# Kernel optimization log

Measured on AMD Instinct MI355X. Metric: run time of the kernel, lower is better.

Reference implementation:

```python
import jax, jax.numpy as jnp
import numpy as np

N_GENE, N_TRAIN, N_EDGES = 20000, 4096, 131072
SRC, DST, H, OUT, NC = 2500, 2675, 2500, 2500, 16
EPS = 1e-5
SLOPE = 0.01  # torch default leaky_relu negative slope


def _leaky(x):
    return jnp.where(x >= 0, x, SLOPE * x)


def _bn(x, g, b):
    # BatchNorm1d, training-mode batch statistics over the node (batch) dim
    m = x.mean(axis=0)
    v = x.var(axis=0)
    return (x - m) * jax.lax.rsqrt(v + EPS) * g + b


def _ln(x, g, b):
    m = x.mean(axis=-1, keepdims=True)
    v = x.var(axis=-1, keepdims=True)
    return (x - m) * jax.lax.rsqrt(v + EPS) * g + b


def _sage(src_f, dst_f, si, di, W_self, W_neigh, b, n_dst):
    # DGL SAGEConv 'mean': fc_self(h_dst) + fc_neigh(mean over in-neighbors)
    msg = src_f[si]                                            # [E, d_src] gather
    agg = jax.ops.segment_sum(msg, di, num_segments=n_dst)     # [n_dst, d_src]
    deg = jax.ops.segment_sum(jnp.ones((si.shape[0],), src_f.dtype), di, num_segments=n_dst)
    mean = agg / jnp.maximum(deg, 1.0)[:, None]
    return dst_f @ W_self + mean @ W_neigh + b


def setup_inputs() -> dict:
    key = jax.random.key(0)
    ks = jax.random.split(key, 20)
    s = 0.02  # weight scale to keep deep 2500-dim chain numerically tame
    n = lambda k, shp: jax.random.normal(k, shp, dtype=jnp.float32)
    return {
        'gene_feats': n(ks[0], (N_GENE, SRC)),
        'train_feats': n(ks[1], (N_TRAIN, DST - NC)),
        'y_hat': n(ks[2], (N_TRAIN, NC)),
        'edge_src': jax.random.randint(ks[3], (N_EDGES,), 0, N_GENE, dtype=jnp.int32),
        'edge_dst': jax.random.randint(ks[4], (N_EDGES,), 0, N_TRAIN, dtype=jnp.int32),
        'W_self3': n(ks[5], (DST, H)) * s, 'W_neigh3': n(ks[6], (SRC, H)) * s, 'b3': jnp.zeros((H,), jnp.float32),
        'bn3_g': jnp.ones((H,), jnp.float32), 'bn3_b': jnp.zeros((H,), jnp.float32),
        'Wq': n(ks[7], (H, H)) * s, 'Wk': n(ks[8], (H, H)) * s, 'Wv': n(ks[9], (H, H)) * s,
        'bq': jnp.zeros((H,), jnp.float32), 'bk': jnp.zeros((H,), jnp.float32), 'bv': jnp.zeros((H,), jnp.float32),
        'Wo': n(ks[10], (H, H)) * s, 'bo': jnp.zeros((H,), jnp.float32),
        'ln2_g': jnp.ones((H,), jnp.float32), 'ln2_b': jnp.zeros((H,), jnp.float32),
        'W_self4': n(ks[11], (H, OUT)) * s, 'W_neigh4': n(ks[12], (SRC, OUT)) * s, 'b4': jnp.zeros((OUT,), jnp.float32),
        'bn4_g': jnp.ones((OUT,), jnp.float32), 'bn4_b': jnp.zeros((OUT,), jnp.float32),
        'W_lin2': n(ks[13], (OUT, OUT)) * s, 'b_lin2': jnp.zeros((OUT,), jnp.float32),
        'W_ce': n(ks[14], (OUT, NC)) * s, 'b_ce': jnp.zeros((NC,), jnp.float32),
    }


def reference(gene_feats, train_feats, y_hat, edge_src, edge_dst,
              W_self3, W_neigh3, b3, bn3_g, bn3_b,
              Wq, Wk, Wv, bq, bk, bv, Wo, bo, ln2_g, ln2_b,
              W_self4, W_neigh4, b4, bn4_g, bn4_b,
              W_lin2, b_lin2, W_ce, b_ce):
    # concat label logits onto train-node features (dst dim -> 2675)
    dst = jnp.concatenate([train_feats, y_hat], axis=1)
    # conv3: bipartite SAGE gene_node -> train_node
    h = _sage(gene_feats, dst, edge_src, edge_dst, W_self3, W_neigh3, b3, N_TRAIN)
    h = _leaky(_bn(h, bn3_g, bn3_b))
    # single-head self-attention over ALL train nodes as one sequence [L=N_TRAIN, E=H]
    q = h @ Wq + bq
    k = h @ Wk + bk
    v = h @ Wv + bv
    attn = jax.nn.softmax(q @ k.T * (1.0 / jnp.sqrt(jnp.asarray(H, h.dtype))), axis=-1)
    h = (attn @ v) @ Wo + bo
    h = _leaky(_ln(h, ln2_g, ln2_b))
    # (dropout omitted: eval-mode identity)
    # conv4: same graph, src = raw gene feats, dst = attention output
    h = _sage(gene_feats, h, edge_src, edge_dst, W_self4, W_neigh4, b4, N_TRAIN)
    x_hat = _leaky(_bn(h, bn4_g, bn4_b))
    y = jax.nn.relu(x_hat @ W_lin2 + b_lin2) @ W_ce + b_ce
    return (x_hat, y)
```

## Files before the change

### kernel.cpp

```cpp
#include <hip/hip_runtime.h>
#include <hip/hip_bf16.h>
#include <cstdint>
#include <cstddef>

constexpr int NTRAIN = 4096;
constexpr int NEDGES = 131072;
constexpr int DSRC = 2500, DH = 2500, DNC = 16;
constexpr int KD1 = 2659;
constexpr int KC3 = 5175;
constexpr int KP3 = 5184;
constexpr int KC4 = 5000;
constexpr int KP4 = 5056;
constexpr int KPH = 2560;
constexpr int NPW = 2560;
constexpr int NQKV = 7680;
constexpr int GSTR = 2504;
constexpr float EPSV = 1e-5f;
constexpr float SLOPEV = 0.01f;

typedef __attribute__((ext_vector_type(8))) short bf16x8;
typedef __attribute__((ext_vector_type(4))) float f32x4;

static __device__ __forceinline__ unsigned short bfbits(float f) {
    __hip_bfloat16 h = __float2bfloat16(f);
    return *reinterpret_cast<unsigned short*>(&h);
}
static __device__ __forceinline__ float b2f(short s) {
    return __uint_as_float(((unsigned)(unsigned short)s) << 16);
}

__global__ void count_deg_k(const int* __restrict__ edst, int* __restrict__ deg) {
    int e = blockIdx.x * 256 + threadIdx.x;
    if (e < NEDGES) atomicAdd(&deg[edst[e]], 1);
}

__global__ __launch_bounds__(1024) void scan_deg_k(const int* __restrict__ deg,
                                                   int* __restrict__ indptr,
                                                   int* __restrict__ cursor) {
    __shared__ int sums[1024];
    int t = threadIdx.x;
    int base = t * 4;
    int d0 = deg[base + 0], d1 = deg[base + 1], d2 = deg[base + 2], d3 = deg[base + 3];
    sums[t] = d0 + d1 + d2 + d3;
    __syncthreads();
    for (int o = 1; o < 1024; o <<= 1) {
        int v = (t >= o) ? sums[t - o] : 0;
        __syncthreads();
        sums[t] += v;
        __syncthreads();
    }
    int excl = (t == 0) ? 0 : sums[t - 1];
    int p0 = excl, p1 = p0 + d0, p2 = p1 + d1, p3 = p2 + d2;
    indptr[base + 0] = p0; indptr[base + 1] = p1; indptr[base + 2] = p2; indptr[base + 3] = p3;
    cursor[base + 0] = p0; cursor[base + 1] = p1; cursor[base + 2] = p2; cursor[base + 3] = p3;
    if (t == 1023) indptr[4096] = p3 + d3;
}

__global__ void scatter_edges_k(const int* __restrict__ esrc, const int* __restrict__ edst,
                                int* __restrict__ cursor, int* __restrict__ csr_src) {
    int e = blockIdx.x * 256 + threadIdx.x;
    if (e < NEDGES) {
        int d = edst[e];
        int p = atomicAdd(&cursor[d], 1);
        csr_src[p] = esrc[e];
    }
}

__global__ __launch_bounds__(256) void gene2bf_k(const float* __restrict__ gene,
                                                 short* __restrict__ gbf) {
    int v = blockIdx.x * 256 + threadIdx.x;
    if (v >= 313) return;
    int row = blockIdx.y;
    const float* src = gene + (size_t)row * DSRC + v * 8;
    f32x4 a = *(const f32x4*)(src);
    f32x4 b = {0.f, 0.f, 0.f, 0.f};
    if (v < 312) b = *(const f32x4*)(src + 4);
    bf16x8 o;
#pragma unroll
    for (int c = 0; c < 4; c++) o[c] = (short)bfbits(a[c]);
#pragma unroll
    for (int c = 0; c < 4; c++) o[4 + c] = (short)bfbits(b[c]);
    *(bf16x8*)(gbf + (size_t)row * GSTR + v * 8) = o;
}

__global__ __launch_bounds__(256) void sage_mean_k(const short* __restrict__ gbf,
                                                   const int* __restrict__ indptr,
                                                   const int* __restrict__ csr_src,
                                                   __hip_bfloat16* __restrict__ A3,
                                                   __hip_bfloat16* __restrict__ A4) {
    int row = blockIdx.x;
    int s = indptr[row], e = indptr[row + 1];
    int t = threadIdx.x;
    float a0[8], a1[8];
#pragma unroll
    for (int c = 0; c < 8; c++) { a0[c] = 0.f; a1[c] = 0.f; }
    bool has1 = (t < 57);
    int j = s;
    for (; j + 2 <= e; j += 2) {
        const bf16x8* g0 = (const bf16x8*)(gbf + (size_t)csr_src[j] * GSTR);
        const bf16x8* g1 = (const bf16x8*)(gbf + (size_t)csr_src[j + 1] * GSTR);
        bf16x8 u0 = g0[t], w0 = g1[t];
        bf16x8 u1, w1;
        if (has1) { u1 = g0[t + 256]; w1 = g1[t + 256]; }
#pragma unroll
        for (int c = 0; c < 8; c++) a0[c] += b2f(u0[c]) + b2f(w0[c]);
        if (has1) {
#pragma unroll
            for (int c = 0; c < 8; c++) a1[c] += b2f(u1[c]) + b2f(w1[c]);
        }
    }
    if (j < e) {
        const bf16x8* g0 = (const bf16x8*)(gbf + (size_t)csr_src[j] * GSTR);
        bf16x8 u0 = g0[t];
#pragma unroll
        for (int c = 0; c < 8; c++) a0[c] += b2f(u0[c]);
        if (has1) {
            bf16x8 u1 = g0[t + 256];
#pragma unroll
            for (int c = 0; c < 8; c++) a1[c] += b2f(u1[c]);
        }
    }
    float inv = 1.f / fmaxf((float)(e - s), 1.f);
#pragma unroll
    for (int c = 0; c < 8; c++) {
        int f = t * 8 + c;
        __hip_bfloat16 h = __float2bfloat16(a0[c] * inv);
        A3[(size_t)row * KP3 + 2675 + f] = h;
        A4[(size_t)row * KP4 + 2500 + f] = h;
    }
    if (has1) {
#pragma unroll
        for (int c = 0; c < 8; c++) {
            int f = (t + 256) * 8 + c;
            if (f < 2500) {
                __hip_bfloat16 h = __float2bfloat16(a1[c] * inv);
                A3[(size_t)row * KP3 + 2675 + f] = h;
                A4[(size_t)row * KP4 + 2500 + f] = h;
            }
        }
    }
}

__global__ void dst_build_k(const float* __restrict__ trainf, const float* __restrict__ yhat,
                            __hip_bfloat16* __restrict__ A3) {
    int c = blockIdx.x * 256 + threadIdx.x;
    int r = blockIdx.y;
    if (c >= KP3) return;
    if (c >= 2675 && c < KC3) return;
    float v = 0.f;
    if (c < KD1) v = trainf[(size_t)r * KD1 + c];
    else if (c < 2675) v = yhat[r * DNC + (c - KD1)];
    A3[(size_t)r * KP3 + c] = __float2bfloat16(v);
}

__global__ __launch_bounds__(256) void wtrans_k(const float* __restrict__ W1,
                                                const float* __restrict__ W2, int ldw,
                                                __hip_bfloat16* __restrict__ Wt,
                                                int Nreal, int K1, int K12, int Kpad, int Npad) {
    __shared__ float tile[32][33];
    int k0 = blockIdx.x * 32, n0 = blockIdx.y * 32;
    int x = threadIdx.x & 31, y = threadIdx.x >> 5;
#pragma unroll
    for (int i = 0; i < 32; i += 8) {
        int k = k0 + y + i, n = n0 + x;
        float v = 0.f;
        if (n < Nreal) {
            if (k < K1) v = W1[(size_t)k * ldw + n];
            else if (k < K12) v = W2[(size_t)(k - K1) * ldw + n];
        }
        tile[y + i][x] = v;
    }
    __syncthreads();
#pragma unroll
    for (int i = 0; i < 32; i += 8) {
        int n = n0 + y + i, k = k0 + x;
        if (n < Npad && k < Kpad) Wt[(size_t)n * Kpad + k] = __float2bfloat16(tile[x][y + i]);
    }
}

__global__ __launch_bounds__(256) void btrans_k(const __hip_bfloat16* __restrict__ V, int ldv,
                                                __hip_bfloat16* __restrict__ VT) {
    __shared__ __hip_bfloat16 tile[32][33];
    int r0 = blockIdx.x * 32, c0 = blockIdx.y * 32;
    int x = threadIdx.x & 31, y = threadIdx.x >> 5;
#pragma unroll
    for (int i = 0; i < 32; i += 8)
        tile[y + i][x] = V[(size_t)(r0 + y + i) * ldv + c0 + x];
    __syncthreads();
#pragma unroll
    for (int i = 0; i < 32; i += 8)
        VT[(size_t)(c0 + y + i) * NTRAIN + r0 + x] = tile[x][y + i];
}

__global__ void qkv_bias_k(const float* __restrict__ bq, const float* __restrict__ bk,
                           const float* __restrict__ bv, float* __restrict__ bqkv) {
    int i = blockIdx.x * 256 + threadIdx.x;
    if (i >= NQKV) return;
    int j = i / KPH, c = i % KPH;
    const float* src = (j == 0) ? bq : (j == 1) ? bk : bv;
    bqkv[i] = (c < DH) ? src[c] : 0.f;
}

__device__ __forceinline__ void async_cp16(const void* g, void* l) {
    __builtin_amdgcn_global_load_lds((const __attribute__((address_space(1))) void*)g,
                                     (__attribute__((address_space(3))) void*)l, 16, 0, 0);
}
#define WAITVM(N) asm volatile("s_waitcnt vmcnt(" #N ")" ::: "memory")
#define LGKM0 asm volatile("s_waitcnt lgkmcnt(0)" ::: "memory")
#define SB __builtin_amdgcn_sched_barrier(0)
static __device__ __forceinline__ void bar_raw() {
    asm volatile("" ::: "memory");
    __builtin_amdgcn_s_barrier();
    asm volatile("" ::: "memory");
}

__global__ __launch_bounds__(512, 2) void gemm256_k(const short* __restrict__ A,
                                                    const short* __restrict__ Bt,
                                                    const float* __restrict__ bias,
                                                    float* __restrict__ Cf,
                                                    __hip_bfloat16* __restrict__ Cb,
                                                    float* __restrict__ psOut,
                                                    float* __restrict__ ps2Out,
                                                    int N, int K, int sA, int sB, int ldc,
                                                    int nmod, float alpha, int act) {
    __shared__ short smem[65536];
    int nwg = gridDim.x * gridDim.y;
    int orig = blockIdx.y * gridDim.x + blockIdx.x;
    int qd = nwg >> 3, rr = nwg & 7;
    int xcd = orig & 7, oidx = orig >> 3;
    int nb = (xcd < rr ? xcd * (qd + 1) : rr * (qd + 1) + (xcd - rr) * qd) + oidx;
    int bx = nb % gridDim.x, by = nb / gridDim.x;
    int row0 = by * 256, col0 = bx * 256;

    int tid = threadIdx.x;
    int wave = tid >> 6, lane = tid & 63;
    int wm = wave >> 2, wn = wave & 3;

    int rsub = lane >> 2;
    int cs = ((lane & 3) * 8) ^ ((lane >= 32) ? 16 : 0);
    const short* gA0 = A + (size_t)(row0 + wave * 16 + rsub) * sA + cs;
    const short* gA1 = A + (size_t)(row0 + wave * 16 + 128 + rsub) * sA + cs;
    const short* gB0 = Bt + (size_t)(col0 + wave * 16 + rsub) * sB + cs;
    const short* gB1 = Bt + (size_t)(col0 + wave * 16 + 128 + rsub) * sB + cs;
    int sa0 = wave * 1024;
    int sa1 = (wave + 8) * 1024;

    int fr = lane & 15, kq = lane >> 4;
    int roff = fr * 32 + ((kq * 8) ^ ((fr & 8) ? 16 : 0));

    f32x4 acc[8][4];
#pragma unroll
    for (int i = 0; i < 8; i++)
#pragma unroll
        for (int j = 0; j < 4; j++)
#pragma unroll
            for (int r = 0; r < 4; r++) acc[i][j][r] = 0.f;

#define STAGE_A(kb, b, k0s) { \
    short* l0 = smem + (b) * 32768 + sa0 + (kb) * 512; \
    short* l1 = smem + (b) * 32768 + sa1 + (kb) * 512; \
    async_cp16(gA0 + (k0s) + (kb) * 32, l0); \
    async_cp16(gA1 + (k0s) + (kb) * 32, l1); }
#define STAGE_B(kb, b, k0s) { \
    short* l0 = smem + (b) * 32768 + 16384 + sa0 + (kb) * 512; \
    short* l1 = smem + (b) * 32768 + 16384 + sa1 + (kb) * 512; \
    async_cp16(gB0 + (k0s) + (kb) * 32, l0); \
    async_cp16(gB1 + (k0s) + (kb) * 32, l1); }
#define DSRA(dst, mq, kk) \
    _Pragma("unroll") for (int i = 0; i < 4; i++) \
        dst[i] = *(const bf16x8*)(ab + (((wm * 8 + (mq) * 4 + i) * 2 + (kk)) << 9) + roff);
#define DSRB(dst, kk) \
    _Pragma("unroll") for (int j = 0; j < 4; j++) \
        dst[j] = *(const bf16x8*)(bb + (((wn * 4 + j) * 2 + (kk)) << 9) + roff);
#define MFMA16(av, bvv, mq) \
    __builtin_amdgcn_s_setprio(1); \
    _Pragma("unroll") for (int i = 0; i < 4; i++) \
        _Pragma("unroll") for (int j = 0; j < 4; j++) \
            acc[(mq) * 4 + i][j] = __builtin_amdgcn_mfma_f32_16x16x32_bf16(av[i], bvv[j], acc[(mq) * 4 + i][j], 0, 0, 0); \
    __builtin_amdgcn_s_setprio(0);

    int nt = K >> 6;
    STAGE_A(0, 0, 0); STAGE_B(0, 0, 0); STAGE_A(1, 0, 0); STAGE_B(1, 0, 0);
    WAITVM(4);
    bar_raw();
    int buf = 0;
    for (int t = 0; t < nt - 1; ++t) {
        const short* ab = smem + (buf << 15);
        const short* bb = ab + 16384;
        int k1 = (t + 1) << 6;
        bf16x8 a0[4], a1[4], b0[4], b1[4];
        DSRA(a0, 0, 0); DSRB(b0, 0);
        STAGE_A(0, buf ^ 1, k1);
        bar_raw(); LGKM0; SB;
        MFMA16(a0, b0, 0);
        SB; bar_raw();
        DSRA(a1, 1, 0);
        STAGE_B(0, buf ^ 1, k1);
        WAITVM(4);
        bar_raw(); LGKM0; SB;
        MFMA16(a1, b0, 1);
        SB; bar_raw();
        DSRA(a0, 0, 1); DSRB(b1, 1);
        STAGE_A(1, buf ^ 1, k1);
        bar_raw(); LGKM0; SB;
        MFMA16(a0, b1, 0);
        SB; bar_raw();
        DSRA(a1, 1, 1);
        STAGE_B(1, buf ^ 1, k1);
        WAITVM(4);
        bar_raw(); LGKM0; SB;
        MFMA16(a1, b1, 1);
        SB; bar_raw();
        buf ^= 1;
    }
    {
        const short* ab = smem + (buf << 15);
        const short* bb = ab + 16384;
        bf16x8 a0[4], a1[4], b0[4], b1[4];
        DSRA(a0, 0, 0); DSRB(b0, 0);
        bar_raw(); LGKM0; SB;
        MFMA16(a0, b0, 0);
        SB; bar_raw();
        DSRA(a1, 1, 0);
        WAITVM(0);
        bar_raw(); LGKM0; SB;
        MFMA16(a1, b0, 1);
        SB; bar_raw();
        DSRA(a0, 0, 1); DSRB(b1, 1);
        bar_raw(); LGKM0; SB;
        MFMA16(a0, b1, 0);
        SB; bar_raw();
        DSRA(a1, 1, 1);
        bar_raw(); LGKM0; SB;
        MFMA16(a1, b1, 1);
        SB;
    }
#undef STAGE_A
#undef STAGE_B
#undef DSRA
#undef DSRB
#undef MFMA16

    int cn = lane & 15, cm = kq * 4;
    int mbase = row0 + wm * 128, nbase = col0 + wn * 64;
    if (Cb) {
#pragma unroll
        for (int j = 0; j < 4; j++) {
            int n = nbase + j * 16 + cn;
            if (n >= ldc) continue;
            bool real = (n % nmod) < N;
            float bvv = (real && bias) ? bias[n] : 0.f;
#pragma unroll
            for (int i = 0; i < 8; i++) {
#pragma unroll
                for (int r = 0; r < 4; r++) {
                    int m = mbase + i * 16 + cm + r;
                    float c = real ? alpha * acc[i][j][r] + bvv : 0.f;
                    if (act) c = fmaxf(c, 0.f);
                    Cb[(size_t)m * ldc + n] = __float2bfloat16(c);
                }
            }
        }
    } else {
#pragma unroll
        for (int j = 0; j < 4; j++) {
            int n = nbase + j * 16 + cn;
            if (n >= N) continue;
            float bvv = bias ? bias[n] : 0.f;
#pragma unroll
            for (int i = 0; i < 8; i++) {
#pragma unroll
                for (int r = 0; r < 4; r++) {
                    int m = mbase + i * 16 + cm + r;
                    float c = alpha * acc[i][j][r] + bvv;
                    if (act) c = fmaxf(c, 0.f);
                    Cf[(size_t)m * ldc + n] = c;
                }
            }
        }
    }
    if (!Cb && psOut) {
        float cs[4], cs2[4];
#pragma unroll
        for (int j = 0; j < 4; j++) { cs[j] = 0.f; cs2[j] = 0.f; }
#pragma unroll
        for (int j = 0; j < 4; j++) {
            int n = nbase + j * 16 + cn;
            if (n >= N) continue;
            float bvv = bias ? bias[n] : 0.f;
#pragma unroll
            for (int i = 0; i < 8; i++) {
#pragma unroll
                for (int r = 0; r < 4; r++) {
                    float c = alpha * acc[i][j][r] + bvv;
                    if (act) c = fmaxf(c, 0.f);
                    cs[j] += c;
                    cs2[j] += c * c;
                }
            }
        }
        bar_raw();
        float* red = (float*)smem;
        int pid = wm * 4 + kq;
#pragma unroll
        for (int j = 0; j < 4; j++) {
            int slot = wn * 64 + j * 16 + cn;
            red[pid * 256 + slot] = cs[j];
            red[2048 + pid * 256 + slot] = cs2[j];
        }
        bar_raw();
        if (wm == 0 && kq == 0) {
#pragma unroll
            for (int j = 0; j < 4; j++) {
                int slot = wn * 64 + j * 16 + cn;
                float s = 0.f, s2 = 0.f;
#pragma unroll
                for (int p = 0; p < 8; p++) {
                    s += red[p * 256 + slot];
                    s2 += red[2048 + p * 256 + slot];
                }
                int n = col0 + slot;
                if (n < N) {
                    psOut[(size_t)by * N + n] = s;
                    ps2Out[(size_t)by * N + n] = s2;
                }
            }
        }
    }
}

__global__ void bn_finalize_k(const float* __restrict__ ps, const float* __restrict__ ps2,
                              const float* __restrict__ g, const float* __restrict__ b,
                              float* __restrict__ scale, float* __restrict__ shift,
                              int Ncol, int nParts, int M) {
    int c = blockIdx.x * 256 + threadIdx.x;
    if (c >= Ncol) return;
    double s = 0, s2 = 0;
    for (int p = 0; p < nParts; p++) {
        s += ps[(size_t)p * Ncol + c];
        s2 += ps2[(size_t)p * Ncol + c];
    }
    double m = s / M;
    double v = s2 / M - m * m;
    float sc = g[c] / sqrtf((float)v + EPSV);
    scale[c] = sc;
    shift[c] = b[c] - (float)m * sc;
}

__global__ void bn_apply_k(const float* __restrict__ X, const float* __restrict__ scale,
                           const float* __restrict__ shift, __hip_bfloat16* __restrict__ Yb,
                           float* __restrict__ Yf, int Nreal, int Cpad) {
    int c = blockIdx.x * 256 + threadIdx.x;
    int r = blockIdx.y;
    if (c >= Cpad) return;
    float v = 0.f;
    if (c < Nreal) {
        v = fmaf(X[(size_t)r * Nreal + c], scale[c], shift[c]);
        v = v >= 0.f ? v : SLOPEV * v;
        if (Yf) Yf[(size_t)r * Nreal + c] = v;
    }
    Yb[(size_t)r * Cpad + c] = __float2bfloat16(v);
}

__device__ __forceinline__ double wave_sum_d(double v) {
#pragma unroll
    for (int o = 32; o > 0; o >>= 1) v += __shfl_down(v, o, 64);
    return v;
}
__device__ __forceinline__ float wave_sum_f(float v) {
#pragma unroll
    for (int o = 32; o > 0; o >>= 1) v += __shfl_down(v, o, 64);
    return v;
}
__device__ __forceinline__ float wave_max_f(float v) {
#pragma unroll
    for (int o = 32; o > 0; o >>= 1) v = fmaxf(v, __shfl_down(v, o, 64));
    return v;
}

__global__ __launch_bounds__(256) void ln_leaky_k(const float* __restrict__ X,
                                                  const float* __restrict__ g,
                                                  const float* __restrict__ b,
                                                  __hip_bfloat16* __restrict__ A4) {
    int row = blockIdx.x;
    const float* xr = X + (size_t)row * DH;
    double s = 0, s2 = 0;
    for (int c = threadIdx.x; c < DH; c += 256) {
        float x = xr[c];
        s += x;
        s2 += (double)x * x;
    }
    __shared__ double sb[4], sb2[4];
    int lane = threadIdx.x & 63, w = threadIdx.x >> 6;
    s = wave_sum_d(s);
    s2 = wave_sum_d(s2);
    if (lane == 0) { sb[w] = s; sb2[w] = s2; }
    __syncthreads();
    double S = sb[0] + sb[1] + sb[2] + sb[3];
    double S2 = sb2[0] + sb2[1] + sb2[2] + sb2[3];
    double m = S / DH;
    double v = S2 / DH - m * m;
    float inv = 1.f / sqrtf((float)v + EPSV);
    float mf = (float)m;
    __hip_bfloat16* yr = A4 + (size_t)row * KP4;
    for (int c = threadIdx.x; c < DH; c += 256) {
        float x = (xr[c] - mf) * inv * g[c] + b[c];
        x = x >= 0.f ? x : SLOPEV * x;
        yr[c] = __float2bfloat16(x);
    }
    if (threadIdx.x < KP4 - KC4) yr[KC4 + threadIdx.x] = __float2bfloat16(0.f);
}

__global__ __launch_bounds__(256) void softmax1_k(const float* __restrict__ X,
                                                  __hip_bfloat16* __restrict__ Y) {
    int row = blockIdx.x, t = threadIdx.x;
    const f32x4* xr = reinterpret_cast<const f32x4*>(X + (size_t)row * NTRAIN);
    f32x4 v[4];
    float mx = -3.4e38f;
#pragma unroll
    for (int i = 0; i < 4; i++) {
        v[i] = xr[i * 256 + t];
#pragma unroll
        for (int c = 0; c < 4; c++) mx = fmaxf(mx, v[i][c]);
    }
    __shared__ float sb[4];
    int lane = t & 63, w = t >> 6;
    mx = wave_max_f(mx);
    if (lane == 0) sb[w] = mx;
    __syncthreads();
    mx = fmaxf(fmaxf(sb[0], sb[1]), fmaxf(sb[2], sb[3]));
    float s = 0.f;
#pragma unroll
    for (int i = 0; i < 4; i++)
#pragma unroll
        for (int c = 0; c < 4; c++) {
            float e = expf(v[i][c] - mx);
            v[i][c] = e;
            s += e;
        }
    s = wave_sum_f(s);
    __syncthreads();
    if (lane == 0) sb[w] = s;
    __syncthreads();
    float inv = 1.f / (sb[0] + sb[1] + sb[2] + sb[3]);
    ushort4* yr = reinterpret_cast<ushort4*>(Y + (size_t)row * NTRAIN);
#pragma unroll
    for (int i = 0; i < 4; i++) {
        ushort4 o;
        o.x = bfbits(v[i][0] * inv);
        o.y = bfbits(v[i][1] * inv);
        o.z = bfbits(v[i][2] * inv);
        o.w = bfbits(v[i][3] * inv);
        yr[i * 256 + t] = o;
    }
}

__global__ __launch_bounds__(256) void head_k(const float* __restrict__ X,
                                              const float* __restrict__ Wce,
                                              const float* __restrict__ bce,
                                              float* __restrict__ Y) {
    int row = blockIdx.x;
    int n = threadIdx.x & 15, part = threadIdx.x >> 4;
    const float* xr = X + (size_t)row * DH;
    float s = 0.f;
    for (int k = part; k < DH; k += 16) s += xr[k] * Wce[k * 16 + n];
    __shared__ float red[256];
    red[threadIdx.x] = s;
    __syncthreads();
    for (int off = 8; off >= 1; off >>= 1) {
        if (part < off) red[threadIdx.x] += red[threadIdx.x + off * 16];
        __syncthreads();
    }
    if (part == 0) Y[row * 16 + n] = red[n] + bce[n];
}

extern "C" void kernel_launch(void* const* d_in, const int* in_sizes, int n_in,
                              void* d_out, int out_size, void* d_ws, size_t ws_size,
                              hipStream_t stream) {
    const float* gene    = (const float*)d_in[0];
    const float* trainf  = (const float*)d_in[1];
    const float* yhat    = (const float*)d_in[2];
    const int*   esrc    = (const int*)d_in[3];
    const int*   edst    = (const int*)d_in[4];
    const float* W_self3 = (const float*)d_in[5];
    const float* W_neigh3= (const float*)d_in[6];
    const float* b3      = (const float*)d_in[7];
    const float* bn3_g   = (const float*)d_in[8];
    const float* bn3_b   = (const float*)d_in[9];
    const float* Wq      = (const float*)d_in[10];
    const float* Wk      = (const float*)d_in[11];
    const float* Wv      = (const float*)d_in[12];
    const float* bq      = (const float*)d_in[13];
    const float* bk      = (const float*)d_in[14];
    const float* bv      = (const float*)d_in[15];
    const float* Wo      = (const float*)d_in[16];
    const float* bo      = (const float*)d_in[17];
    const float* ln2_g   = (const float*)d_in[18];
    const float* ln2_b   = (const float*)d_in[19];
    const float* W_self4 = (const float*)d_in[20];
    const float* W_neigh4= (const float*)d_in[21];
    const float* b4      = (const float*)d_in[22];
    const float* bn4_g   = (const float*)d_in[23];
    const float* bn4_b   = (const float*)d_in[24];
    const float* W_lin2  = (const float*)d_in[25];
    const float* b_lin2  = (const float*)d_in[26];
    const float* W_ce    = (const float*)d_in[27];
    const float* b_ce    = (const float*)d_in[28];

    char* ws = (char*)d_ws;
    size_t off = 0;
    auto alloc = [&](size_t bytes) -> void* {
        void* p = ws + off;
        off = (off + bytes + 255) & ~(size_t)255;
        return p;
    };
    __hip_bfloat16* A3cat  = (__hip_bfloat16*)alloc((size_t)NTRAIN * KP3 * 2);
    __hip_bfloat16* A4cat  = (__hip_bfloat16*)alloc((size_t)NTRAIN * KP4 * 2);
    __hip_bfloat16* h_bf   = (__hip_bfloat16*)alloc((size_t)NTRAIN * KPH * 2);
    __hip_bfloat16* qkv_bf = (__hip_bfloat16*)alloc((size_t)NTRAIN * NQKV * 2);
    __hip_bfloat16* W3t    = (__hip_bfloat16*)alloc((size_t)NPW * KP3 * 2);
    __hip_bfloat16* Wqkvt  = (__hip_bfloat16*)alloc((size_t)3 * NPW * KPH * 2);
    float*  bigC   = (float*)alloc((size_t)NTRAIN * NTRAIN * 4);
    float*  ps     = (float*)alloc((size_t)16 * DH * 4);
    float*  ps2    = (float*)alloc((size_t)16 * DH * 4);
    float*  scale  = (float*)alloc(DH * 4);
    float*  shift  = (float*)alloc(DH * 4);
    float*  bqkv   = (float*)alloc(NQKV * 4);
    int*    deg    = (int*)alloc(NTRAIN * 4);
    int*    indptr = (int*)alloc((NTRAIN + 1) * 4);
    int*    cursor = (int*)alloc(NTRAIN * 4);
    int*    csr_src= (int*)alloc(NEDGES * 4);
    __hip_bfloat16* attn_bf = A3cat;
    __hip_bfloat16* W4t     = W3t;
    __hip_bfloat16* Wot     = Wqkvt;
    __hip_bfloat16* Wlin2t  = Wqkvt;
    __hip_bfloat16* xhat_bf = h_bf;
    __hip_bfloat16* ao_bf   = qkv_bf;
    __hip_bfloat16* vT_bf   = (__hip_bfloat16*)bigC;
    short* gene_bf = (short*)W3t;

    float* xhat = (float*)d_out;
    float* yout = (float*)d_out + (size_t)NTRAIN * DH;

    auto gemm = [&](const void* A, const void* Bt, const float* bias, float* Cf,
                    __hip_bfloat16* Cb, float* psO, float* ps2O, int NpadCols, int Nreal,
                    int K, int sA, int sB, int ldc, int nmod, float alpha, int act) {
        dim3 g(NpadCols / 256, NTRAIN / 256);
        gemm256_k<<<g, 512, 0, stream>>>((const short*)A, (const short*)Bt, bias, Cf, Cb,
                                         psO, ps2O, Nreal, K, sA, sB, ldc, nmod, alpha, act);
    };

    hipMemsetAsync(deg, 0, NTRAIN * 4, stream);
    count_deg_k<<<NEDGES / 256, 256, 0, stream>>>(edst, deg);
    scan_deg_k<<<1, 1024, 0, stream>>>(deg, indptr, cursor);
    scatter_edges_k<<<NEDGES / 256, 256, 0, stream>>>(esrc, edst, cursor, csr_src);
    gene2bf_k<<<dim3(2, 20000), 256, 0, stream>>>(gene, gene_bf);
    sage_mean_k<<<NTRAIN, 256, 0, stream>>>(gene_bf, indptr, csr_src, A3cat, A4cat);
    dst_build_k<<<dim3((KP3 + 255) / 256, NTRAIN), 256, 0, stream>>>(trainf, yhat, A3cat);
    wtrans_k<<<dim3(KP3 / 32, NPW / 32), 256, 0, stream>>>(W_self3, W_neigh3, DH, W3t, DH, 2675, KC3, KP3, NPW);

    gemm(A3cat, W3t, b3, bigC, nullptr, ps, ps2, NPW, DH, KP3, KP3, KP3, DH, DH, 1.f, 0);
    bn_finalize_k<<<(DH + 255) / 256, 256, 0, stream>>>(ps, ps2, bn3_g, bn3_b, scale, shift, DH, 16, NTRAIN);
    bn_apply_k<<<dim3((KPH + 255) / 256, NTRAIN), 256, 0, stream>>>(bigC, scale, shift, h_bf, nullptr, DH, KPH);

    wtrans_k<<<dim3(KPH / 32, NPW / 32), 256, 0, stream>>>(Wq, nullptr, DH, Wqkvt, DH, DH, DH, KPH, NPW);
    wtrans_k<<<dim3(KPH / 32, NPW / 32), 256, 0, stream>>>(Wk, nullptr, DH, Wqkvt + (size_t)NPW * KPH, DH, DH, DH, KPH, NPW);
    wtrans_k<<<dim3(KPH / 32, NPW / 32), 256, 0, stream>>>(Wv, nullptr, DH, Wqkvt + (size_t)2 * NPW * KPH, DH, DH, DH, KPH, NPW);
    qkv_bias_k<<<NQKV / 256, 256, 0, stream>>>(bq, bk, bv, bqkv);
    gemm(h_bf, Wqkvt, bqkv, nullptr, qkv_bf, nullptr, nullptr, NQKV, DH, KPH, KPH, KPH, NQKV, KPH, 1.f, 0);
    gemm(qkv_bf, qkv_bf + KPH, nullptr, bigC, nullptr, nullptr, nullptr, NTRAIN, NTRAIN, KPH, NQKV, NQKV, NTRAIN, NTRAIN, 0.02f, 0);
    softmax1_k<<<NTRAIN, 256, 0, stream>>>(bigC, attn_bf);
    btrans_k<<<dim3(NTRAIN / 32, KPH / 32), 256, 0, stream>>>(qkv_bf + 2 * KPH, NQKV, vT_bf);
    gemm(attn_bf, vT_bf, nullptr, nullptr, ao_bf, nullptr, nullptr, NPW, DH, NTRAIN, NTRAIN, NTRAIN, KPH, KPH, 1.f, 0);
    wtrans_k<<<dim3(KPH / 32, NPW / 32), 256, 0, stream>>>(Wo, nullptr, DH, Wot, DH, DH, DH, KPH, NPW);
    gemm(ao_bf, Wot, bo, bigC, nullptr, nullptr, nullptr, NPW, DH, KPH, KPH, KPH, DH, DH, 1.f, 0);
    ln_leaky_k<<<NTRAIN, 256, 0, stream>>>(bigC, ln2_g, ln2_b, A4cat);

    wtrans_k<<<dim3(KP4 / 32, NPW / 32), 256, 0, stream>>>(W_self4, W_neigh4, DH, W4t, DH, DH, KC4, KP4, NPW);
    gemm(A4cat, W4t, b4, bigC, nullptr, ps, ps2, NPW, DH, KP4, KP4, KP4, DH, DH, 1.f, 0);
    bn_finalize_k<<<(DH + 255) / 256, 256, 0, stream>>>(ps, ps2, bn4_g, bn4_b, scale, shift, DH, 16, NTRAIN);
    bn_apply_k<<<dim3((KPH + 255) / 256, NTRAIN), 256, 0, stream>>>(bigC, scale, shift, xhat_bf, xhat, DH, KPH);

    wtrans_k<<<dim3(KPH / 32, NPW / 32), 256, 0, stream>>>(W_lin2, nullptr, DH, Wlin2t, DH, DH, DH, KPH, NPW);
    gemm(xhat_bf, Wlin2t, b_lin2, bigC, nullptr, nullptr, nullptr, NPW, DH, KPH, KPH, KPH, DH, DH, 1.f, 1);
    head_k<<<NTRAIN, 256, 0, stream>>>(bigC, W_ce, b_ce, yout);
    (void)ws_size; (void)n_in; (void)in_sizes; (void)out_size;
}
```

Baseline: 1.674 ms.

## Fold weight transposes into preceding GEMM launches as extra workgroups

The separate weight-transpose/bf16-convert kernels (Wq/Wk/Wv, Wo, W4, W_lin2) are removed. Their work now runs as extra workgroups appended to an earlier, independent GEMM launch. Those blocks take a branch at kernel entry and do tiled transposes through LDS. This is meant to remove launch overhead and let the transposes fill the GEMM tail. The risks are more kernel arguments, possible register or occupancy effects, and the need for the aliased scratch buffers to be free when they are written.

```diff
diff --git a/kernel.cpp b/kernel.cpp
--- a/kernel.cpp
+++ b/kernel.cpp
@@ -222,10 +222,54 @@
                                                     float* __restrict__ psOut,
                                                     float* __restrict__ ps2Out,
                                                     int N, int K, int sA, int sB, int ldc,
-                                                    int nmod, float alpha, int act) {
+                                                    int nmod, float alpha, int act,
+                                                    int ngemm,
+                                                    const float* xs0, const float* xs1,
+                                                    const float* xs2, const float* xs3,
+                                                    const float* xs4, const float* xs5,
+                                                    short* xout, long xstride,
+                                                    int xldw, int xNreal, int xK1, int xK12,
+                                                    int xKpad, int xNpad, int nslab) {
     __shared__ short smem[65536];
-    int nwg = gridDim.x * gridDim.y;
+    int nwgt = gridDim.x * gridDim.y;
     int orig = blockIdx.y * gridDim.x + blockIdx.x;
+
+    if (orig >= ngemm) {
+        int wid = orig - ngemm, nw = nwgt - ngemm;
+        float* tile = (float*)smem;
+        int tid = threadIdx.x;
+        int x = tid & 31, y0 = tid >> 5;
+        int ntx = xKpad >> 5, nty = xNpad >> 5;
+        int per = ntx * nty, total = nslab * per;
+        for (int t = wid; t < total; t += nw) {
+            int sl = t / per, rem = t - sl * per;
+            int tx = rem % ntx, ty = rem / ntx;
+            const float* W1 = (sl == 0) ? xs0 : (sl == 1) ? xs2 : xs4;
+            const float* W2 = (sl == 0) ? xs1 : (sl == 1) ? xs3 : xs5;
+            short* out = xout + (size_t)sl * xstride;
+            int k0 = tx * 32, n0 = ty * 32;
+            __syncthreads();
+#pragma unroll
+            for (int i = 0; i < 32; i += 16) {
+                int k = k0 + y0 + i, n = n0 + x;
+                float v = 0.f;
+                if (n < xNreal) {
+                    if (k < xK1) v = W1[(size_t)k * xldw + n];
+                    else if (k < xK12) v = W2[(size_t)(k - xK1) * xldw + n];
+                }
+                tile[(y0 + i) * 33 + x] = v;
+            }
+            __syncthreads();
+#pragma unroll
+            for (int i = 0; i < 32; i += 16) {
+                int n = n0 + y0 + i, k = k0 + x;
+                out[(size_t)n * xKpad + k] = (short)bfbits(tile[x * 33 + y0 + i]);
+            }
+        }
+        return;
+    }
+
+    int nwg = ngemm;
     int qd = nwg >> 3, rr = nwg & 7;
     int xcd = orig & 7, oidx = orig >> 3;
     int nb = (xcd < rr ? xcd * (qd + 1) : rr * (qd + 1) + (xcd - rr) * qd) + oidx;
@@ -380,9 +424,9 @@
         }
     }
     if (!Cb && psOut) {
-        float cs[4], cs2[4];
-#pragma unroll
-        for (int j = 0; j < 4; j++) { cs[j] = 0.f; cs2[j] = 0.f; }
+        float cs2v[4], cs1v[4];
+#pragma unroll
+        for (int j = 0; j < 4; j++) { cs1v[j] = 0.f; cs2v[j] = 0.f; }
 #pragma unroll
         for (int j = 0; j < 4; j++) {
             int n = nbase + j * 16 + cn;
@@ -394,8 +438,8 @@
                 for (int r = 0; r < 4; r++) {
                     float c = alpha * acc[i][j][r] + bvv;
                     if (act) c = fmaxf(c, 0.f);
-                    cs[j] += c;
-                    cs2[j] += c * c;
+                    cs1v[j] += c;
+                    cs2v[j] += c * c;
                 }
             }
         }
@@ -405,8 +449,8 @@
 #pragma unroll
         for (int j = 0; j < 4; j++) {
             int slot = wn * 64 + j * 16 + cn;
-            red[pid * 256 + slot] = cs[j];
-            red[2048 + pid * 256 + slot] = cs2[j];
+            red[pid * 256 + slot] = cs1v[j];
+            red[2048 + pid * 256 + slot] = cs2v[j];
         }
         bar_raw();
         if (wm == 0 && kq == 0) {
@@ -644,11 +688,20 @@
 
     auto gemm = [&](const void* A, const void* Bt, const float* bias, float* Cf,
                     __hip_bfloat16* Cb, float* psO, float* ps2O, int NpadCols, int Nreal,
-                    int K, int sA, int sB, int ldc, int nmod, float alpha, int act) {
-        dim3 g(NpadCols / 256, NTRAIN / 256);
+                    int K, int sA, int sB, int ldc, int nmod, float alpha, int act,
+                    const float* x0, const float* x1, const float* x2, const float* x3,
+                    const float* x4, const float* x5, short* xout, long xstride,
+                    int xldw, int xNreal, int xK1, int xK12, int xKpad, int xNpad, int nslab) {
+        int gx = NpadCols / 256, gy = NTRAIN / 256;
+        int ngemm = gx * gy;
+        int extraY = (nslab > 0) ? 9 : 0;
+        dim3 g(gx, gy + extraY);
         gemm256_k<<<g, 512, 0, stream>>>((const short*)A, (const short*)Bt, bias, Cf, Cb,
-                                         psO, ps2O, Nreal, K, sA, sB, ldc, nmod, alpha, act);
+                                         psO, ps2O, Nreal, K, sA, sB, ldc, nmod, alpha, act,
+                                         ngemm, x0, x1, x2, x3, x4, x5, xout, xstride,
+                                         xldw, xNreal, xK1, xK12, xKpad, xNpad, nslab);
     };
+    const float* Z = nullptr;
 
     hipMemsetAsync(deg, 0, NTRAIN * 4, stream);
     count_deg_k<<<NEDGES / 256, 256, 0, stream>>>(edst, deg);
@@ -659,30 +712,31 @@
     dst_build_k<<<dim3((KP3 + 255) / 256, NTRAIN), 256, 0, stream>>>(trainf, yhat, A3cat);
     wtrans_k<<<dim3(KP3 / 32, NPW / 32), 256, 0, stream>>>(W_self3, W_neigh3, DH, W3t, DH, 2675, KC3, KP3, NPW);
 
-    gemm(A3cat, W3t, b3, bigC, nullptr, ps, ps2, NPW, DH, KP3, KP3, KP3, DH, DH, 1.f, 0);
+    gemm(A3cat, W3t, b3, bigC, nullptr, ps, ps2, NPW, DH, KP3, KP3, KP3, DH, DH, 1.f, 0,
+         Wq, Z, Wk, Z, Wv, Z, (short*)Wqkvt, (long)NPW * KPH, DH, DH, DH, DH, KPH, NPW, 3);
     bn_finalize_k<<<(DH + 255) / 256, 256, 0, stream>>>(ps, ps2, bn3_g, bn3_b, scale, shift, DH, 16, NTRAIN);
     bn_apply_k<<<dim3((KPH + 255) / 256, NTRAIN), 256, 0, stream>>>(bigC, scale, shift, h_bf, nullptr, DH, KPH);
 
-    wtrans_k<<<dim3(KPH / 32, NPW / 32), 256, 0, stream>>>(Wq, nullptr, DH, Wqkvt, DH, DH, DH, KPH, NPW);
-    wtrans_k<<<dim3(KPH / 32, NPW / 32), 256, 0, stream>>>(Wk, nullptr, DH, Wqkvt + (size_t)NPW * KPH, DH, DH, DH, KPH, NPW);
-    wtrans_k<<<dim3(KPH / 32, NPW / 32), 256, 0, stream>>>(Wv, nullptr, DH, Wqkvt + (size_t)2 * NPW * KPH, DH, DH, DH, KPH, NPW);
     qkv_bias_k<<<NQKV / 256, 256, 0, stream>>>(bq, bk, bv, bqkv);
-    gemm(h_bf, Wqkvt, bqkv, nullptr, qkv_bf, nullptr, nullptr, NQKV, DH, KPH, KPH, KPH, NQKV, KPH, 1.f, 0);
-    gemm(qkv_bf, qkv_bf + KPH, nullptr, bigC, nullptr, nullptr, nullptr, NTRAIN, NTRAIN, KPH, NQKV, NQKV, NTRAIN, NTRAIN, 0.02f, 0);
+    gemm(h_bf, Wqkvt, bqkv, nullptr, qkv_bf, nullptr, nullptr, NQKV, DH, KPH, KPH, KPH, NQKV, KPH, 1.f, 0,
+         Z, Z, Z, Z, Z, Z, nullptr, 0, 0, 0, 0, 0, 32, 32, 0);
+    gemm(qkv_bf, qkv_bf + KPH, nullptr, bigC, nullptr, nullptr, nullptr, NTRAIN, NTRAIN, KPH, NQKV, NQKV, NTRAIN, NTRAIN, 0.02f, 0,
+         Z, Z, Z, Z, Z, Z, nullptr, 0, 0, 0, 0, 0, 32, 32, 0);
     softmax1_k<<<NTRAIN, 256, 0, stream>>>(bigC, attn_bf);
     btrans_k<<<dim3(NTRAIN / 32, KPH / 32), 256, 0, stream>>>(qkv_bf + 2 * KPH, NQKV, vT_bf);
-    gemm(attn_bf, vT_bf, nullptr, nullptr, ao_bf, nullptr, nullptr, NPW, DH, NTRAIN, NTRAIN, NTRAIN, KPH, KPH, 1.f, 0);
-    wtrans_k<<<dim3(KPH / 32, NPW / 32), 256, 0, stream>>>(Wo, nullptr, DH, Wot, DH, DH, DH, KPH, NPW);
-    gemm(ao_bf, Wot, bo, bigC, nullptr, nullptr, nullptr, NPW, DH, KPH, KPH, KPH, DH, DH, 1.f, 0);
+    gemm(attn_bf, vT_bf, nullptr, nullptr, ao_bf, nullptr, nullptr, NPW, DH, NTRAIN, NTRAIN, NTRAIN, KPH, KPH, 1.f, 0,
+         Wo, Z, Z, Z, Z, Z, (short*)Wot, 0, DH, DH, DH, DH, KPH, NPW, 1);
+    gemm(ao_bf, Wot, bo, bigC, nullptr, nullptr, nullptr, NPW, DH, KPH, KPH, KPH, DH, DH, 1.f, 0,
+         W_self4, W_neigh4, Z, Z, Z, Z, (short*)W4t, 0, DH, DH, DH, KC4, KP4, NPW, 1);
     ln_leaky_k<<<NTRAIN, 256, 0, stream>>>(bigC, ln2_g, ln2_b, A4cat);
 
-    wtrans_k<<<dim3(KP4 / 32, NPW / 32), 256, 0, stream>>>(W_self4, W_neigh4, DH, W4t, DH, DH, KC4, KP4, NPW);
-    gemm(A4cat, W4t, b4, bigC, nullptr, ps, ps2, NPW, DH, KP4, KP4, KP4, DH, DH, 1.f, 0);
+    gemm(A4cat, W4t, b4, bigC, nullptr, ps, ps2, NPW, DH, KP4, KP4, KP4, DH, DH, 1.f, 0,
+         W_lin2, Z, Z, Z, Z, Z, (short*)Wlin2t, 0, DH, DH, DH, DH, KPH, NPW, 1);
     bn_finalize_k<<<(DH + 255) / 256, 256, 0, stream>>>(ps, ps2, bn4_g, bn4_b, scale, shift, DH, 16, NTRAIN);
     bn_apply_k<<<dim3((KPH + 255) / 256, NTRAIN), 256, 0, stream>>>(bigC, scale, shift, xhat_bf, xhat, DH, KPH);
 
-    wtrans_k<<<dim3(KPH / 32, NPW / 32), 256, 0, stream>>>(W_lin2, nullptr, DH, Wlin2t, DH, DH, DH, KPH, NPW);
-    gemm(xhat_bf, Wlin2t, b_lin2, bigC, nullptr, nullptr, nullptr, NPW, DH, KPH, KPH, KPH, DH, DH, 1.f, 1);
+    gemm(xhat_bf, Wlin2t, b_lin2, bigC, nullptr, nullptr, nullptr, NPW, DH, KPH, KPH, KPH, DH, DH, 1.f, 1,
+         Z, Z, Z, Z, Z, Z, nullptr, 0, 0, 0, 0, 0, 32, 32, 0);
     head_k<<<NTRAIN, 256, 0, stream>>>(bigC, W_ce, b_ce, yout);
     (void)ws_size; (void)n_in; (void)in_sizes; (void)out_size;
 }
```

New measurement: 1.909 ms. +14.0%, slower.
